# Optimization experiments

Measured on AMD Instinct MI355X. Metric: run time of the kernel, lower is better.

## Reference

```python
import jax, jax.numpy as jnp
import numpy as np

FIELDS = 39
FEATURE_DIMS = 100000
EMB = 16


def setup_inputs() -> dict:
    key = jax.random.key(0)
    k1, k2 = jax.random.split(key)
    X = jax.random.randint(k1, (4096, FIELDS), 0, FEATURE_DIMS, dtype=jnp.int32)
    table = jax.random.normal(k2, (FEATURE_DIMS, FIELDS, EMB), dtype=jnp.float32) * 0.05
    return {"X": X, "table": table}


def reference(X, table):
    # FFM field-aware interaction, strict upper triangle of field pairs.
    # Original builds full [B,F,F,D] product then masks; math per pair (i<j):
    #   out[b,p,d] = table[X[b,i], j, d] * table[X[b,j], i, d]
    F = FIELDS
    iu, ju = np.triu_indices(F, k=1)          # P = F*(F-1)//2 pairs
    left = table[X[:, iu], ju]                # [B, P, D]
    right = table[X[:, ju], iu]               # [B, P, D]
    return left * right
```

## Files before the change

### kernel.cpp

```cpp
#include <hip/hip_runtime.h>
#include <math.h>


#define F        39
#define NPAIR    741
#define ROWF4    (F * 4)
#define NF4      (F * ROWF4)
#define ROWSH    628
#define OUTF4    (NPAIR * 4)
#define BLK      1024

typedef float fx4 __attribute__((ext_vector_type(4)));

__device__ __forceinline__ unsigned short f32_to_bf16_rne(float f) {
    union { float f; unsigned int i; } c;
    c.f = f;
    const unsigned int r = c.i + 0x7FFFu + ((c.i >> 16) & 1u);
    return (unsigned short)(r >> 16);
}

__device__ __forceinline__ float bf16_to_f32(unsigned short u) {
    union { unsigned int i; float f; } c;
    c.i = ((unsigned int)u) << 16;
    return c.f;
}

__global__ __launch_bounds__(BLK) void ffm_interact_kernel(
    const int* __restrict__ X,
    const fx4* __restrict__ table4,
    fx4*       __restrict__ out4)
{
    __shared__ unsigned short rowsh[F * ROWSH];
    __shared__ int xrow[F];
    __shared__ int loff[NPAIR];
    __shared__ int roff[NPAIR];

    const int b   = blockIdx.x;
    const int tid = threadIdx.x;

    if (tid < F) xrow[tid] = X[b * F + tid];

    if (tid < NPAIR) {
        const int p = tid;
        int i = (int)((77.0f - sqrtf(5929.0f - 8.0f * (float)p)) * 0.5f);
        i = i < 0 ? 0 : (i > 38 ? 38 : i);
        while (((i + 1) * (77 - (i + 1))) / 2 <= p) ++i;
        while ((i * (77 - i)) / 2 > p) --i;
        const int j = p - (i * (77 - i)) / 2 + i + 1;
        loff[p] = i * ROWSH + j * 16;
        roff[p] = j * ROWSH + i * 16;
    }
    __syncthreads();

    for (int idx = tid; idx < NF4; idx += BLK) {
        const int f = idx / ROWF4;
        const int w = idx - f * ROWF4;
        const fx4 v = table4[(size_t)xrow[f] * ROWF4 + w];
        ushort4 h;
        h.x = f32_to_bf16_rne(v.x);
        h.y = f32_to_bf16_rne(v.y);
        h.z = f32_to_bf16_rne(v.z);
        h.w = f32_to_bf16_rne(v.w);
        *(ushort4*)&rowsh[f * ROWSH + w * 4] = h;
    }
    __syncthreads();

    fx4* __restrict__ ob = out4 + (size_t)b * OUTF4;
    for (int o = tid; o < OUTF4; o += BLK) {
        const int p = o >> 2;
        const int e = o & 3;
        const ushort4 L = *(const ushort4*)&rowsh[loff[p] + e * 4];
        const ushort4 R = *(const ushort4*)&rowsh[roff[p] + e * 4];
        fx4 v;
        v.x = bf16_to_f32(L.x) * bf16_to_f32(R.x);
        v.y = bf16_to_f32(L.y) * bf16_to_f32(R.y);
        v.z = bf16_to_f32(L.z) * bf16_to_f32(R.z);
        v.w = bf16_to_f32(L.w) * bf16_to_f32(R.w);
        __builtin_nontemporal_store(v, ob + o);
    }
}

extern "C" void kernel_launch(void* const* d_in, const int* in_sizes, int n_in,
                              void* d_out, int out_size, void* d_ws, size_t ws_size,
                              hipStream_t stream) {
    const int*   X     = (const int*)d_in[0];
    const float* table = (const float*)d_in[1];
    float*       out   = (float*)d_out;

    const int batch = in_sizes[0] / F;

    ffm_interact_kernel<<<dim3(batch), dim3(BLK), 0, stream>>>(
        X, (const fx4*)table, (fx4*)out);
}
```

Measured before the change: 403.1 us.

## Drop shared-memory bf16 staging and gather table rows directly per pair

The kernel no longer stages each sample's 39 table rows into LDS as bf16. Each output vector now loads its left and right fp32 values straight from the global table, using precomputed per-pair base offsets. The block size drops to 512 with an unrolled fixed-count output loop, and the launch bound now asks for higher occupancy. This removes the LDS staging pass, its conversions and one barrier, and also restores full fp32 precision. The cost is that each table element is read from global memory twice, relying on the cache to absorb the repeats.

```diff
diff --git a/kernel.cpp b/kernel.cpp
--- a/kernel.cpp
+++ b/kernel.cpp
@@ -2,81 +2,58 @@
 #include <math.h>
 
 
-#define F        39
-#define NPAIR    741
-#define ROWF4    (F * 4)
-#define NF4      (F * ROWF4)
-#define ROWSH    628
-#define OUTF4    (NPAIR * 4)
-#define BLK      1024
+#define F      39
+#define NPAIR  741
+#define ROWF4  (F * 4)
+#define OUTF4  (NPAIR * 4)
+#define BLK    512
+#define NITER  6
 
 typedef float fx4 __attribute__((ext_vector_type(4)));
 
-__device__ __forceinline__ unsigned short f32_to_bf16_rne(float f) {
-    union { float f; unsigned int i; } c;
-    c.f = f;
-    const unsigned int r = c.i + 0x7FFFu + ((c.i >> 16) & 1u);
-    return (unsigned short)(r >> 16);
-}
-
-__device__ __forceinline__ float bf16_to_f32(unsigned short u) {
-    union { unsigned int i; float f; } c;
-    c.i = ((unsigned int)u) << 16;
-    return c.f;
-}
-
-__global__ __launch_bounds__(BLK) void ffm_interact_kernel(
+__global__ __launch_bounds__(BLK, 4) void ffm_direct_kernel(
     const int* __restrict__ X,
     const fx4* __restrict__ table4,
     fx4*       __restrict__ out4)
 {
-    __shared__ unsigned short rowsh[F * ROWSH];
-    __shared__ int xrow[F];
-    __shared__ int loff[NPAIR];
-    __shared__ int roff[NPAIR];
+    __shared__ int  xrow[F];
+    __shared__ int2 base2[NPAIR];
 
     const int b   = blockIdx.x;
     const int tid = threadIdx.x;
 
     if (tid < F) xrow[tid] = X[b * F + tid];
+    __syncthreads();
 
-    if (tid < NPAIR) {
-        const int p = tid;
+    for (int p = tid; p < NPAIR; p += BLK) {
         int i = (int)((77.0f - sqrtf(5929.0f - 8.0f * (float)p)) * 0.5f);
         i = i < 0 ? 0 : (i > 38 ? 38 : i);
         while (((i + 1) * (77 - (i + 1))) / 2 <= p) ++i;
         while ((i * (77 - i)) / 2 > p) --i;
         const int j = p - (i * (77 - i)) / 2 + i + 1;
-        loff[p] = i * ROWSH + j * 16;
-        roff[p] = j * ROWSH + i * 16;
-    }
-    __syncthreads();
-
-    for (int idx = tid; idx < NF4; idx += BLK) {
-        const int f = idx / ROWF4;
-        const int w = idx - f * ROWF4;
-        const fx4 v = table4[(size_t)xrow[f] * ROWF4 + w];
-        ushort4 h;
-        h.x = f32_to_bf16_rne(v.x);
-        h.y = f32_to_bf16_rne(v.y);
-        h.z = f32_to_bf16_rne(v.z);
-        h.w = f32_to_bf16_rne(v.w);
-        *(ushort4*)&rowsh[f * ROWSH + w * 4] = h;
+        base2[p] = make_int2(xrow[i] * ROWF4 + j * 4,
+                             xrow[j] * ROWF4 + i * 4);
     }
     __syncthreads();
 
     fx4* __restrict__ ob = out4 + (size_t)b * OUTF4;
-    for (int o = tid; o < OUTF4; o += BLK) {
-        const int p = o >> 2;
-        const int e = o & 3;
-        const ushort4 L = *(const ushort4*)&rowsh[loff[p] + e * 4];
-        const ushort4 R = *(const ushort4*)&rowsh[roff[p] + e * 4];
-        fx4 v;
-        v.x = bf16_to_f32(L.x) * bf16_to_f32(R.x);
-        v.y = bf16_to_f32(L.y) * bf16_to_f32(R.y);
-        v.z = bf16_to_f32(L.z) * bf16_to_f32(R.z);
-        v.w = bf16_to_f32(L.w) * bf16_to_f32(R.w);
-        __builtin_nontemporal_store(v, ob + o);
+
+    #pragma unroll
+    for (int k = 0; k < NITER; ++k) {
+        const int o = tid + k * BLK;
+        if (k < NITER - 1 || o < OUTF4) {
+            const int p = o >> 2;
+            const int e = o & 3;
+            const int2 ba = base2[p];
+            const fx4 L = table4[ba.x + e];
+            const fx4 R = table4[ba.y + e];
+            fx4 v;
+            v.x = L.x * R.x;
+            v.y = L.y * R.y;
+            v.z = L.z * R.z;
+            v.w = L.w * R.w;
+            __builtin_nontemporal_store(v, ob + o);
+        }
     }
 }
 
@@ -89,6 +66,6 @@
 
     const int batch = in_sizes[0] / F;
 
-    ffm_interact_kernel<<<dim3(batch), dim3(BLK), 0, stream>>>(
+    ffm_direct_kernel<<<dim3(batch), dim3(BLK), 0, stream>>>(
         X, (const fx4*)table, (fx4*)out);
 }
```

Measured after the change: 405.2 us. Within noise of the previous version (+0.5%).
